# Kernel tuning notes

Measured on AMD Instinct MI355X. Metric: run time of the kernel, lower is better.

Reference implementation:

```python
import jax, jax.numpy as jnp
import numpy as np

D_IN = 1024
D_OUT = 1024


def setup_inputs() -> dict:
    key = jax.random.key(0)
    kx, kq, kk, kv = jax.random.split(key, 4)
    x = jax.random.normal(kx, (4, 2048, D_IN), dtype=jnp.float32)
    s = 1.0 / np.sqrt(D_IN)
    Wq = jax.random.normal(kq, (D_IN, D_OUT), dtype=jnp.float32) * s
    Wk = jax.random.normal(kk, (D_IN, D_OUT), dtype=jnp.float32) * s
    Wv = jax.random.normal(kv, (D_IN, D_OUT), dtype=jnp.float32) * s
    return {"x": x, "Wq": Wq, "Wk": Wk, "Wv": Wv}


def reference(x, Wq, Wk, Wv):
    # x: [B, S, d_in]; W*: [d_in, d_out]
    B, S, _ = x.shape
    q = x @ Wq  # [B, S, d_out]
    k = x @ Wk
    v = x @ Wv
    scale = 1.0 / jnp.sqrt(jnp.asarray(k.shape[-1], x.dtype))
    scores = jnp.einsum("bqd,bkd->bqk", q, k) * scale  # [B, S, S]
    # causal mask: positions j > i masked to -inf (triu, diagonal=1)
    causal = jnp.tril(jnp.ones((S, S), dtype=bool))
    scores = jnp.where(causal[None, :, :], scores, -jnp.inf)
    attn = jax.nn.softmax(scores, axis=-1)  # dropout p=0.0 -> identity
    return jnp.einsum("bqk,bkd->bqd", attn, v)
```

## Files before the change

### kernel.cpp

```cpp
#include <hip/hip_runtime.h>
#include <hip/hip_bf16.h>

#define NB 4
#define SB 2048
#define DD 1024
#define BM 128
#define BN 128
#define BK 32

typedef __attribute__((ext_vector_type(8))) short bf16x8;
typedef __attribute__((ext_vector_type(4))) float f32x4;
typedef unsigned int u32;

__device__ __forceinline__ float bf2f(unsigned short u) {
    return __uint_as_float(((u32)u) << 16);
}
__device__ __forceinline__ short f2bf(float f) {
    u32 u = __float_as_uint(f);
    u32 r = (u + 0x7fffu + ((u >> 16) & 1u)) >> 16;
    return (short)r;
}

__global__ __launch_bounds__(256) void prep(
    const float* __restrict__ x, const float* __restrict__ Wq,
    const float* __restrict__ Wk, const float* __restrict__ Wv,
    short* __restrict__ xb, short* __restrict__ Wt)
{
    __shared__ short t[64][65];
    const int bx = blockIdx.x;
    const int tid = threadIdx.x;
    if (bx < 4096) {
        const size_t i = ((size_t)bx * 256 + tid) * 8;
        float4 a = *(const float4*)&x[i];
        float4 b = *(const float4*)&x[i + 4];
        bf16x8 o;
        o[0] = f2bf(a.x); o[1] = f2bf(a.y); o[2] = f2bf(a.z); o[3] = f2bf(a.w);
        o[4] = f2bf(b.x); o[5] = f2bf(b.y); o[6] = f2bf(b.z); o[7] = f2bf(b.w);
        *(bf16x8*)&xb[i] = o;
        return;
    }
    const int idx = bx - 4096;
    const int z = idx >> 8;
    const int rr = idx & 255;
    const int k0 = (rr & 15) * 64;
    const int n0 = (rr >> 4) * 64;
    const float* W = (z == 0) ? Wq : (z == 1) ? Wk : Wv;
    short* T = Wt + (size_t)z * DD * DD;
    {
        const int r = tid >> 4;
        const int c = (tid & 15) * 4;
#pragma unroll
        for (int i = 0; i < 4; i++) {
            float4 v = *(const float4*)&W[(size_t)(k0 + i * 16 + r) * DD + n0 + c];
            t[i * 16 + r][c + 0] = f2bf(v.x);
            t[i * 16 + r][c + 1] = f2bf(v.y);
            t[i * 16 + r][c + 2] = f2bf(v.z);
            t[i * 16 + r][c + 3] = f2bf(v.w);
        }
    }
    __syncthreads();
    {
        const int r = tid >> 3;
        const int c = (tid & 7) * 8;
#pragma unroll
        for (int i = 0; i < 2; i++) {
            bf16x8 o;
#pragma unroll
            for (int j = 0; j < 8; j++) o[j] = t[c + j][i * 32 + r];
            *(bf16x8*)&T[(size_t)(n0 + i * 32 + r) * DD + k0 + c] = o;
        }
    }
}

__global__ __launch_bounds__(256) void transpose_v(const short* __restrict__ V,
                                                   short* __restrict__ Vt)
{
    __shared__ short t[64][65];
    const int b = blockIdx.z;
    const int s0 = blockIdx.x * 64;
    const int d0 = blockIdx.y * 64;
    const short* Vb = V + (size_t)b * SB * DD;
    short* Tb = Vt + (size_t)b * DD * SB;
    const int tid = threadIdx.x;
    const int r = tid >> 3;
    const int c = (tid & 7) * 8;
#pragma unroll
    for (int i = 0; i < 2; i++) {
        bf16x8 v = *(const bf16x8*)&Vb[(size_t)(s0 + i * 32 + r) * DD + d0 + c];
#pragma unroll
        for (int j = 0; j < 8; j++) t[i * 32 + r][c + j] = v[j];
    }
    __syncthreads();
#pragma unroll
    for (int i = 0; i < 2; i++) {
        bf16x8 o;
#pragma unroll
        for (int j = 0; j < 8; j++) o[j] = t[c + j][i * 32 + r];
        *(bf16x8*)&Tb[(size_t)(d0 + i * 32 + r) * SB + s0 + c] = o;
    }
}

__device__ __forceinline__ void stage128x32(const short* __restrict__ g, int ld,
                                            short* lds, int tid) {
    const int wave = tid >> 6, lane = tid & 63;
    const int r = lane >> 2;
    const int c = (lane & 3) * 8;
#pragma unroll
    for (int i = 0; i < 2; i++) {
        const int chunk = wave * 2 + i;
        const short* gp = g + (size_t)(chunk * 16 + r) * ld + c;
        __builtin_amdgcn_global_load_lds(
            (const __attribute__((address_space(1))) u32*)gp,
            (__attribute__((address_space(3))) u32*)(lds + chunk * 512 + lane * 8),
            16, 0, 0);
    }
}

__device__ __forceinline__ void gemm_bt_body(
    const short* __restrict__ A, int lda, const short* __restrict__ Bt, int ldb,
    int m0, int n0, int kend, short* As, short* Bs, f32x4 (&acc)[4][4], int tid)
{
    const int lane = tid & 63;
    const int wave = tid >> 6;
    const int wm = (wave >> 1) * 64, wn = (wave & 1) * 64;
    const int fr = lane & 15;
    const int quad = lane >> 4;
    for (int k0 = 0; k0 < kend; k0 += BK) {
        stage128x32(A + (size_t)m0 * lda + k0, lda, As, tid);
        stage128x32(Bt + (size_t)n0 * ldb + k0, ldb, Bs, tid);
        __syncthreads();
        bf16x8 af[4], bf[4];
#pragma unroll
        for (int t = 0; t < 4; t++) {
            af[t] = *(const bf16x8*)&As[(wm + t * 16 + fr) * BK + quad * 8];
            bf[t] = *(const bf16x8*)&Bs[(wn + t * 16 + fr) * BK + quad * 8];
        }
#pragma unroll
        for (int mt = 0; mt < 4; mt++)
#pragma unroll
            for (int nt = 0; nt < 4; nt++)
                acc[mt][nt] = __builtin_amdgcn_mfma_f32_16x16x32_bf16(
                    af[mt], bf[nt], acc[mt][nt], 0, 0, 0);
        __syncthreads();
    }
}

__global__ __launch_bounds__(256) void qkv_mfma(
    const short* __restrict__ xb, const short* __restrict__ Wt,
    short* __restrict__ Q, short* __restrict__ K, short* __restrict__ V)
{
    __shared__ short As[BM * BK], Bs[BN * BK];
    const int n0 = blockIdx.x * BN;
    const int m0 = blockIdx.y * BM;
    const int z = blockIdx.z;
    const short* B = Wt + (size_t)z * DD * DD;
    short* C = (z == 0) ? Q : (z == 1) ? K : V;
    f32x4 acc[4][4];
#pragma unroll
    for (int a = 0; a < 4; a++)
#pragma unroll
        for (int b = 0; b < 4; b++) acc[a][b] = (f32x4){0.f, 0.f, 0.f, 0.f};
    gemm_bt_body(xb, DD, B, DD, m0, n0, DD, As, Bs, acc, threadIdx.x);
    const int lane = threadIdx.x & 63, wave = threadIdx.x >> 6;
    const int wm = (wave >> 1) * 64, wn = (wave & 1) * 64;
    const int fr = lane & 15, quad = lane >> 4;
#pragma unroll
    for (int mt = 0; mt < 4; mt++)
#pragma unroll
        for (int nt = 0; nt < 4; nt++)
#pragma unroll
            for (int r = 0; r < 4; r++) {
                const size_t m = m0 + wm + mt * 16 + quad * 4 + r;
                const size_t n = n0 + wn + nt * 16 + fr;
                C[m * DD + n] = f2bf(acc[mt][nt][r]);
            }
}

__global__ __launch_bounds__(256) void scores_mfma(
    const short* __restrict__ Q, const short* __restrict__ Kc,
    short* __restrict__ Sc)
{
    const int idx = blockIdx.x;
    int qt = (int)((__fsqrt_rn(8.f * idx + 1.f) - 1.f) * 0.5f);
    while ((qt + 1) * (qt + 2) / 2 <= idx) qt++;
    while (qt * (qt + 1) / 2 > idx) qt--;
    const int kt = idx - qt * (qt + 1) / 2;
    const int qm0 = qt * BM;
    const int kn0 = kt * BN;
    const int b = blockIdx.y;
    __shared__ short As[BM * BK], Bs[BN * BK];
    const short* Qb = Q + (size_t)b * SB * DD;
    const short* Kb = Kc + (size_t)b * SB * DD;
    short* Sb = Sc + (size_t)b * SB * SB;
    f32x4 acc[4][4];
#pragma unroll
    for (int a = 0; a < 4; a++)
#pragma unroll
        for (int c = 0; c < 4; c++) acc[a][c] = (f32x4){0.f, 0.f, 0.f, 0.f};
    gemm_bt_body(Qb, DD, Kb, DD, qm0, kn0, DD, As, Bs, acc, threadIdx.x);
    const int lane = threadIdx.x & 63, wave = threadIdx.x >> 6;
    const int wm = (wave >> 1) * 64, wn = (wave & 1) * 64;
    const int fr = lane & 15, quad = lane >> 4;
    const float scale = 0.03125f;
#pragma unroll
    for (int mt = 0; mt < 4; mt++)
#pragma unroll
        for (int nt = 0; nt < 4; nt++)
#pragma unroll
            for (int r = 0; r < 4; r++) {
                const size_t q = qm0 + wm + mt * 16 + quad * 4 + r;
                const size_t k = kn0 + wn + nt * 16 + fr;
                Sb[q * SB + k] = f2bf(acc[mt][nt][r] * scale);
            }
}

__global__ __launch_bounds__(256) void softmax_kernel(short* __restrict__ Sc)
{
    const int row = blockIdx.x;
    const int i = row & (SB - 1);
    const int jlim = ((i >> 7) + 1) << 7;
    short* r = Sc + (size_t)row * SB;
    const int t = threadIdx.x;
    const int lane = t & 63, wave = t >> 6;
    __shared__ float red[8];

    float v[8];
    float mx = -1e30f;
#pragma unroll
    for (int c = 0; c < 8; c++) {
        const int j = c * 256 + t;
        const float s = (j <= i) ? bf2f((unsigned short)r[j]) : -1e30f;
        v[c] = s;
        mx = fmaxf(mx, s);
    }
#pragma unroll
    for (int o = 32; o > 0; o >>= 1) mx = fmaxf(mx, __shfl_down(mx, o));
    if (lane == 0) red[wave] = mx;
    __syncthreads();
    mx = fmaxf(fmaxf(red[0], red[1]), fmaxf(red[2], red[3]));

    float sum = 0.f;
#pragma unroll
    for (int c = 0; c < 8; c++) {
        const int j = c * 256 + t;
        const float e = (j <= i) ? __expf(v[c] - mx) : 0.f;
        v[c] = e;
        sum += e;
    }
#pragma unroll
    for (int o = 32; o > 0; o >>= 1) sum += __shfl_down(sum, o);
    if (lane == 0) red[4 + wave] = sum;
    __syncthreads();
    const float inv = 1.0f / (red[4] + red[5] + red[6] + red[7]);
#pragma unroll
    for (int c = 0; c < 8; c++) {
        const int j = c * 256 + t;
        if (j < jlim) r[j] = f2bf(v[c] * inv);
    }
}

__global__ __launch_bounds__(256) void pv_mfma(
    const short* __restrict__ P, const short* __restrict__ Vt,
    float* __restrict__ O, float* __restrict__ Pp)
{
    __shared__ short As[BM * BK], Bs[BN * BK];
    const int n0 = blockIdx.x * BN;
    const int y = blockIdx.y;
    const int chunk1 = (y >= 16);
    const int qt = chunk1 ? (y - 8) : y;
    const int qm0 = qt * BM;
    const int kstart = chunk1 ? 1024 : 0;
    const int kstop = chunk1 ? (qt + 1) * BM : min(1024, (qt + 1) * BM);
    const int b = blockIdx.z;
    const short* Pb = P + (size_t)b * SB * SB + kstart;
    const short* Vb = Vt + (size_t)b * DD * SB + kstart;
    f32x4 acc[4][4];
#pragma unroll
    for (int a = 0; a < 4; a++)
#pragma unroll
        for (int c = 0; c < 4; c++) acc[a][c] = (f32x4){0.f, 0.f, 0.f, 0.f};
    gemm_bt_body(Pb, SB, Vb, SB, qm0, n0, kstop - kstart, As, Bs, acc,
                 threadIdx.x);
    const int lane = threadIdx.x & 63, wave = threadIdx.x >> 6;
    const int wm = (wave >> 1) * 64, wn = (wave & 1) * 64;
    const int fr = lane & 15, quad = lane >> 4;
    float* dst = chunk1 ? (Pp + (size_t)b * 1024 * DD - (size_t)1024 * DD)
                        : (O + (size_t)b * SB * DD);
    if (chunk1) dst = Pp + (size_t)b * 1024 * DD;
    const int qoff = chunk1 ? 1024 : 0;
#pragma unroll
    for (int mt = 0; mt < 4; mt++)
#pragma unroll
        for (int nt = 0; nt < 4; nt++)
#pragma unroll
            for (int r = 0; r < 4; r++) {
                const size_t q = qm0 + wm + mt * 16 + quad * 4 + r - qoff;
                const size_t n = n0 + wn + nt * 16 + fr;
                dst[q * DD + n] = acc[mt][nt][r];
            }
}

__global__ __launch_bounds__(256) void reduce_pv(const float* __restrict__ Pp,
                                                 float* __restrict__ O)
{
    const size_t e = ((size_t)blockIdx.x * 256 + threadIdx.x) * 4;
    const size_t b = e / ((size_t)1024 * DD);
    const size_t rem = e - b * (size_t)1024 * DD;
    float4 p = *(const float4*)&Pp[e];
    float* o = &O[b * (size_t)SB * DD + (size_t)1024 * DD + rem];
    float4 v = *(const float4*)o;
    v.x += p.x; v.y += p.y; v.z += p.z; v.w += p.w;
    *(float4*)o = v;
}

extern "C" void kernel_launch(void* const* d_in, const int* in_sizes, int n_in,
                              void* d_out, int out_size, void* d_ws, size_t ws_size,
                              hipStream_t stream)
{
    const float* x  = (const float*)d_in[0];
    const float* Wq = (const float*)d_in[1];
    const float* Wk = (const float*)d_in[2];
    const float* Wv = (const float*)d_in[3];
    float* out = (float*)d_out;

    const size_t QKV_ELEMS = (size_t)NB * SB * DD;
    short* Q  = (short*)d_ws;
    short* K  = Q + QKV_ELEMS;
    short* Vt = K + QKV_ELEMS;
    char*  R  = (char*)(Vt + QKV_ELEMS);
    short* V  = (short*)R;
    short* xb = V + QKV_ELEMS;
    short* Wt = xb + QKV_ELEMS;
    short* Sc = (short*)R;
    float* Pp = (float*)(Sc + (size_t)NB * SB * SB);

    prep<<<dim3(4096 + 768), 256, 0, stream>>>(x, Wq, Wk, Wv, xb, Wt);
    qkv_mfma<<<dim3(DD / BN, (NB * SB) / BM, 3), 256, 0, stream>>>(xb, Wt, Q, K, V);
    transpose_v<<<dim3(SB / 64, DD / 64, NB), 256, 0, stream>>>(V, Vt);
    scores_mfma<<<dim3(136, NB), 256, 0, stream>>>(Q, K, Sc);
    softmax_kernel<<<dim3(NB * SB), 256, 0, stream>>>(Sc);
    pv_mfma<<<dim3(DD / BN, 24, NB), 256, 0, stream>>>(Sc, Vt, out, Pp);
    reduce_pv<<<dim3((unsigned)((size_t)NB * 1024 * DD / 4 / 256)), 256, 0,
                stream>>>(Pp, out);
}
```

Before: 270.7 us.

## Fold Wq·Wkᵀ into one matrix and compute scores as (xM)·xᵀ

Precomputes M = Wq·Wkᵀ once (a 1024³ GEMM), then forms T = x·M and scores as T·xᵀ. This removes the separate K projection, one of three 8192×1024×1024 GEMMs, at the cost of a smaller 1024² GEMM. The V projection now writes its output transposed directly from the GEMM epilogue, which eliminates the transpose_v kernel and its extra pass over memory. The workspace layout is rearranged, and rounding M to bf16 adds some numerical error.

Result: no change. 271.3 us (+0.2%).

```diff
diff --git a/kernel.cpp b/kernel.cpp
--- a/kernel.cpp
+++ b/kernel.cpp
@@ -9,6 +9,7 @@
 #define BK 32
 
 typedef __attribute__((ext_vector_type(8))) short bf16x8;
+typedef __attribute__((ext_vector_type(4))) short bf16x4;
 typedef __attribute__((ext_vector_type(4))) float f32x4;
 typedef unsigned int u32;
 
@@ -24,34 +25,42 @@
 __global__ __launch_bounds__(256) void prep(
     const float* __restrict__ x, const float* __restrict__ Wq,
     const float* __restrict__ Wk, const float* __restrict__ Wv,
-    short* __restrict__ xb, short* __restrict__ Wt)
+    short* __restrict__ xb, short* __restrict__ Wqb,
+    short* __restrict__ Wkb, short* __restrict__ Wvt)
 {
     __shared__ short t[64][65];
     const int bx = blockIdx.x;
     const int tid = threadIdx.x;
-    if (bx < 4096) {
-        const size_t i = ((size_t)bx * 256 + tid) * 8;
-        float4 a = *(const float4*)&x[i];
-        float4 b = *(const float4*)&x[i + 4];
+    if (bx < 5120) {
+        const float* src;
+        short* dst;
+        size_t i;
+        if (bx < 4096) {
+            src = x; dst = xb;
+            i = ((size_t)bx * 256 + tid) * 8;
+        } else {
+            const int w = bx - 4096;
+            src = (w < 512) ? Wq : Wk;
+            dst = (w < 512) ? Wqb : Wkb;
+            i = ((size_t)(w & 511) * 256 + tid) * 8;
+        }
+        float4 a = *(const float4*)&src[i];
+        float4 b = *(const float4*)&src[i + 4];
         bf16x8 o;
         o[0] = f2bf(a.x); o[1] = f2bf(a.y); o[2] = f2bf(a.z); o[3] = f2bf(a.w);
         o[4] = f2bf(b.x); o[5] = f2bf(b.y); o[6] = f2bf(b.z); o[7] = f2bf(b.w);
-        *(bf16x8*)&xb[i] = o;
+        *(bf16x8*)&dst[i] = o;
         return;
     }
-    const int idx = bx - 4096;
-    const int z = idx >> 8;
-    const int rr = idx & 255;
+    const int rr = bx - 5120;
     const int k0 = (rr & 15) * 64;
     const int n0 = (rr >> 4) * 64;
-    const float* W = (z == 0) ? Wq : (z == 1) ? Wk : Wv;
-    short* T = Wt + (size_t)z * DD * DD;
     {
         const int r = tid >> 4;
         const int c = (tid & 15) * 4;
 #pragma unroll
         for (int i = 0; i < 4; i++) {
-            float4 v = *(const float4*)&W[(size_t)(k0 + i * 16 + r) * DD + n0 + c];
+            float4 v = *(const float4*)&Wv[(size_t)(k0 + i * 16 + r) * DD + n0 + c];
             t[i * 16 + r][c + 0] = f2bf(v.x);
             t[i * 16 + r][c + 1] = f2bf(v.y);
             t[i * 16 + r][c + 2] = f2bf(v.z);
@@ -67,36 +76,8 @@
             bf16x8 o;
 #pragma unroll
             for (int j = 0; j < 8; j++) o[j] = t[c + j][i * 32 + r];
-            *(bf16x8*)&T[(size_t)(n0 + i * 32 + r) * DD + k0 + c] = o;
+            *(bf16x8*)&Wvt[(size_t)(n0 + i * 32 + r) * DD + k0 + c] = o;
         }
-    }
-}
-
-__global__ __launch_bounds__(256) void transpose_v(const short* __restrict__ V,
-                                                   short* __restrict__ Vt)
-{
-    __shared__ short t[64][65];
-    const int b = blockIdx.z;
-    const int s0 = blockIdx.x * 64;
-    const int d0 = blockIdx.y * 64;
-    const short* Vb = V + (size_t)b * SB * DD;
-    short* Tb = Vt + (size_t)b * DD * SB;
-    const int tid = threadIdx.x;
-    const int r = tid >> 3;
-    const int c = (tid & 7) * 8;
-#pragma unroll
-    for (int i = 0; i < 2; i++) {
-        bf16x8 v = *(const bf16x8*)&Vb[(size_t)(s0 + i * 32 + r) * DD + d0 + c];
-#pragma unroll
-        for (int j = 0; j < 8; j++) t[i * 32 + r][c + j] = v[j];
-    }
-    __syncthreads();
-#pragma unroll
-    for (int i = 0; i < 2; i++) {
-        bf16x8 o;
-#pragma unroll
-        for (int j = 0; j < 8; j++) o[j] = t[c + j][i * 32 + r];
-        *(bf16x8*)&Tb[(size_t)(d0 + i * 32 + r) * SB + s0 + c] = o;
     }
 }
 
@@ -145,16 +126,44 @@
     }
 }
 
-__global__ __launch_bounds__(256) void qkv_mfma(
-    const short* __restrict__ xb, const short* __restrict__ Wt,
-    short* __restrict__ Q, short* __restrict__ K, short* __restrict__ V)
+__global__ __launch_bounds__(256) void mm_kernel(
+    const short* __restrict__ Wkb, const short* __restrict__ Wqb,
+    short* __restrict__ Mp)
+{
+    __shared__ short As[BM * BK], Bs[BN * BK];
+    const int n0 = blockIdx.x * BN;
+    const int m0 = blockIdx.y * BM;
+    f32x4 acc[4][4];
+#pragma unroll
+    for (int a = 0; a < 4; a++)
+#pragma unroll
+        for (int b = 0; b < 4; b++) acc[a][b] = (f32x4){0.f, 0.f, 0.f, 0.f};
+    gemm_bt_body(Wkb, DD, Wqb, DD, m0, n0, DD, As, Bs, acc, threadIdx.x);
+    const int lane = threadIdx.x & 63, wave = threadIdx.x >> 6;
+    const int wm = (wave >> 1) * 64, wn = (wave & 1) * 64;
+    const int fr = lane & 15, quad = lane >> 4;
+#pragma unroll
+    for (int mt = 0; mt < 4; mt++)
+#pragma unroll
+        for (int nt = 0; nt < 4; nt++)
+#pragma unroll
+            for (int r = 0; r < 4; r++) {
+                const size_t m = m0 + wm + mt * 16 + quad * 4 + r;
+                const size_t n = n0 + wn + nt * 16 + fr;
+                Mp[m * DD + n] = f2bf(acc[mt][nt][r]);
+            }
+}
+
+__global__ __launch_bounds__(256) void tv_gemm(
+    const short* __restrict__ xb, const short* __restrict__ Mp,
+    const short* __restrict__ Wvt, short* __restrict__ T,
+    short* __restrict__ Vt)
 {
     __shared__ short As[BM * BK], Bs[BN * BK];
     const int n0 = blockIdx.x * BN;
     const int m0 = blockIdx.y * BM;
     const int z = blockIdx.z;
-    const short* B = Wt + (size_t)z * DD * DD;
-    short* C = (z == 0) ? Q : (z == 1) ? K : V;
+    const short* B = (z == 0) ? Mp : Wvt;
     f32x4 acc[4][4];
 #pragma unroll
     for (int a = 0; a < 4; a++)
@@ -164,20 +173,37 @@
     const int lane = threadIdx.x & 63, wave = threadIdx.x >> 6;
     const int wm = (wave >> 1) * 64, wn = (wave & 1) * 64;
     const int fr = lane & 15, quad = lane >> 4;
-#pragma unroll
-    for (int mt = 0; mt < 4; mt++)
-#pragma unroll
-        for (int nt = 0; nt < 4; nt++)
-#pragma unroll
-            for (int r = 0; r < 4; r++) {
-                const size_t m = m0 + wm + mt * 16 + quad * 4 + r;
+    if (z == 0) {
+#pragma unroll
+        for (int mt = 0; mt < 4; mt++)
+#pragma unroll
+            for (int nt = 0; nt < 4; nt++)
+#pragma unroll
+                for (int r = 0; r < 4; r++) {
+                    const size_t m = m0 + wm + mt * 16 + quad * 4 + r;
+                    const size_t n = n0 + wn + nt * 16 + fr;
+                    T[m * DD + n] = f2bf(acc[mt][nt][r]);
+                }
+    } else {
+        const int bb = m0 >> 11;
+        const int s0 = (m0 & (SB - 1)) + wm + quad * 4;
+        short* Vb = Vt + (size_t)bb * DD * SB;
+#pragma unroll
+        for (int mt = 0; mt < 4; mt++)
+#pragma unroll
+            for (int nt = 0; nt < 4; nt++) {
                 const size_t n = n0 + wn + nt * 16 + fr;
-                C[m * DD + n] = f2bf(acc[mt][nt][r]);
+                const size_t s = s0 + mt * 16;
+                bf16x4 o;
+#pragma unroll
+                for (int r = 0; r < 4; r++) o[r] = f2bf(acc[mt][nt][r]);
+                *(bf16x4*)&Vb[n * SB + s] = o;
             }
+    }
 }
 
 __global__ __launch_bounds__(256) void scores_mfma(
-    const short* __restrict__ Q, const short* __restrict__ Kc,
+    const short* __restrict__ T, const short* __restrict__ xb,
     short* __restrict__ Sc)
 {
     const int idx = blockIdx.x;
@@ -189,15 +215,15 @@
     const int kn0 = kt * BN;
     const int b = blockIdx.y;
     __shared__ short As[BM * BK], Bs[BN * BK];
-    const short* Qb = Q + (size_t)b * SB * DD;
-    const short* Kb = Kc + (size_t)b * SB * DD;
+    const short* Tb = T + (size_t)b * SB * DD;
+    const short* Xb = xb + (size_t)b * SB * DD;
     short* Sb = Sc + (size_t)b * SB * SB;
     f32x4 acc[4][4];
 #pragma unroll
     for (int a = 0; a < 4; a++)
 #pragma unroll
         for (int c = 0; c < 4; c++) acc[a][c] = (f32x4){0.f, 0.f, 0.f, 0.f};
-    gemm_bt_body(Qb, DD, Kb, DD, qm0, kn0, DD, As, Bs, acc, threadIdx.x);
+    gemm_bt_body(Tb, DD, Xb, DD, qm0, kn0, DD, As, Bs, acc, threadIdx.x);
     const int lane = threadIdx.x & 63, wave = threadIdx.x >> 6;
     const int wm = (wave >> 1) * 64, wn = (wave & 1) * 64;
     const int fr = lane & 15, quad = lane >> 4;
@@ -284,9 +310,8 @@
     const int lane = threadIdx.x & 63, wave = threadIdx.x >> 6;
     const int wm = (wave >> 1) * 64, wn = (wave & 1) * 64;
     const int fr = lane & 15, quad = lane >> 4;
-    float* dst = chunk1 ? (Pp + (size_t)b * 1024 * DD - (size_t)1024 * DD)
+    float* dst = chunk1 ? (Pp + (size_t)b * 1024 * DD)
                         : (O + (size_t)b * SB * DD);
-    if (chunk1) dst = Pp + (size_t)b * 1024 * DD;
     const int qoff = chunk1 ? 1024 : 0;
 #pragma unroll
     for (int mt = 0; mt < 4; mt++)
@@ -323,21 +348,24 @@
     const float* Wv = (const float*)d_in[3];
     float* out = (float*)d_out;
 
-    const size_t QKV_ELEMS = (size_t)NB * SB * DD;
-    short* Q  = (short*)d_ws;
-    short* K  = Q + QKV_ELEMS;
-    short* Vt = K + QKV_ELEMS;
-    char*  R  = (char*)(Vt + QKV_ELEMS);
-    short* V  = (short*)R;
-    short* xb = V + QKV_ELEMS;
-    short* Wt = xb + QKV_ELEMS;
-    short* Sc = (short*)R;
-    float* Pp = (float*)(Sc + (size_t)NB * SB * SB);
-
-    prep<<<dim3(4096 + 768), 256, 0, stream>>>(x, Wq, Wk, Wv, xb, Wt);
-    qkv_mfma<<<dim3(DD / BN, (NB * SB) / BM, 3), 256, 0, stream>>>(xb, Wt, Q, K, V);
-    transpose_v<<<dim3(SB / 64, DD / 64, NB), 256, 0, stream>>>(V, Vt);
-    scores_mfma<<<dim3(136, NB), 256, 0, stream>>>(Q, K, Sc);
+    const size_t XE = (size_t)NB * SB * DD;
+    const size_t WE = (size_t)DD * DD;
+    short* xb  = (short*)d_ws;
+    short* T   = xb + XE;
+    short* Vt  = T + XE;
+    short* Sc  = Vt + XE;
+    float* Pp  = (float*)(Sc + (size_t)NB * SB * SB);
+    short* Wqb = (short*)(Pp + (size_t)NB * 1024 * DD);
+    short* Wkb = Wqb + WE;
+    short* Wvt = Wkb + WE;
+    short* Mp  = Wvt + WE;
+
+    prep<<<dim3(4096 + 1024 + 256), 256, 0, stream>>>(
+        x, Wq, Wk, Wv, xb, Wqb, Wkb, Wvt);
+    mm_kernel<<<dim3(DD / BN, DD / BM), 256, 0, stream>>>(Wkb, Wqb, Mp);
+    tv_gemm<<<dim3(DD / BN, (NB * SB) / BM, 2), 256, 0, stream>>>(
+        xb, Mp, Wvt, T, Vt);
+    scores_mfma<<<dim3(136, NB), 256, 0, stream>>>(T, xb, Sc);
     softmax_kernel<<<dim3(NB * SB), 256, 0, stream>>>(Sc);
     pv_mfma<<<dim3(DD / BN, 24, NB), 256, 0, stream>>>(Sc, Vt, out, Pp);
     reduce_pv<<<dim3((unsigned)((size_t)NB * 1024 * DD / 4 / 256)), 256, 0,
```
